# Kernel tuning notes

Measured on AMD Instinct MI355X. Metric: run time of the kernel, lower is better.

The kernel has to match this reference:

```python
import jax, jax.numpy as jnp
import numpy as np

N_NODES = 100000


def _deg_norm(idx, n):
    # inverse-sqrt degree, zero-degree nodes -> 0 (DGL norm='both' convention)
    deg = jax.ops.segment_sum(jnp.ones(idx.shape, jnp.float32), idx, num_segments=n)
    return jnp.where(deg > 0, jax.lax.rsqrt(jnp.maximum(deg, 1.0)), 0.0)


def graph_conv(x, src, dst, W, b, n):
    # symmetric normalization: D_out^{-1/2} on src, D_in^{-1/2} on dst
    norm_src = _deg_norm(src, n)  # [N]
    norm_dst = _deg_norm(dst, n)  # [N]
    h = (x * norm_src[:, None]) @ W          # apply weight first (in >= out)
    msg = h[src]                              # gather [E, out]
    agg = jax.ops.segment_sum(msg, dst, num_segments=n)  # scatter-add [N, out]
    return agg * norm_dst[:, None] + b


def setup_inputs() -> dict:
    key = jax.random.key(0)
    ks = jax.random.split(key, 6)
    x = jax.random.normal(ks[0], (N_NODES, 128), dtype=jnp.float32)
    edge_index = jax.random.randint(ks[1], (2, 1600000), 0, N_NODES, dtype=jnp.int64)
    W1 = jax.random.normal(ks[2], (128, 64), dtype=jnp.float32) * (1.0 / np.sqrt(128))
    b1 = jnp.zeros((64,), jnp.float32)
    W2 = jax.random.normal(ks[3], (64, 32), dtype=jnp.float32) * (1.0 / np.sqrt(64))
    b2 = jnp.zeros((32,), jnp.float32)
    Wl = jax.random.normal(ks[4], (32, 1), dtype=jnp.float32) * (1.0 / np.sqrt(32))
    bl = jnp.zeros((1,), jnp.float32)
    return {"x": x, "edge_index": edge_index, "W1": W1, "b1": b1,
            "W2": W2, "b2": b2, "Wl": Wl, "bl": bl}


def reference(x, edge_index, W1, b1, W2, b2, Wl, bl):
    src, dst = edge_index[0], edge_index[1]
    n = x.shape[0]
    h = graph_conv(x, src, dst, W1, b1, n)
    h = jax.nn.relu(h)
    # dropout(p=0.5) is identity at inference
    h = graph_conv(h, src, dst, W2, b2, n)
    return h @ Wl + bl  # [N, 1]
```

## Files before the change

kernel.cpp:

```cpp
#include <hip/hip_runtime.h>
#include <hip/hip_fp16.h>


#define WAVE 64
#define NRANGE 8

__global__ __launch_bounds__(256) void k_hist(const int* __restrict__ srcArr,
                                              const int* __restrict__ dstArr,
                                              unsigned* __restrict__ partial_s,
                                              unsigned* __restrict__ partial_d,
                                              int E, int B, int C, int chunkE) {
    extern __shared__ unsigned hist[];
    const int r = blockIdx.x & (NRANGE - 1);
    const int c = blockIdx.x >> 3;
    const int lo = r * B;
    const int* nodes = blockIdx.y ? dstArr : srcArr;
    unsigned* partial = blockIdx.y ? partial_d : partial_s;

    for (int b = threadIdx.x; b < B; b += 256) hist[b] = 0u;
    __syncthreads();

    const int beg = c * chunkE, end = min(beg + chunkE, E);
    const int n4 = (end - beg) >> 2;
    const int4* p = (const int4*)(nodes + beg);
    for (int j = threadIdx.x; j < n4; j += 256) {
        int4 v = p[j];
        int a;
        a = v.x - lo; if ((unsigned)a < (unsigned)B) atomicAdd(&hist[a], 1u);
        a = v.y - lo; if ((unsigned)a < (unsigned)B) atomicAdd(&hist[a], 1u);
        a = v.z - lo; if ((unsigned)a < (unsigned)B) atomicAdd(&hist[a], 1u);
        a = v.w - lo; if ((unsigned)a < (unsigned)B) atomicAdd(&hist[a], 1u);
    }
    for (int j = beg + (n4 << 2) + threadIdx.x; j < end; j += 256) {
        int a = nodes[j] - lo;
        if ((unsigned)a < (unsigned)B) atomicAdd(&hist[a], 1u);
    }
    __syncthreads();
    unsigned* outp = partial + (size_t)(r * C + c) * B;
    for (int b = threadIdx.x; b < B; b += 256) outp[b] = hist[b];
}

__global__ __launch_bounds__(256) void k_reduce_norm(const unsigned* __restrict__ partial_s,
                                                     unsigned* __restrict__ partial_d,
                                                     float* __restrict__ norm_s,
                                                     float* __restrict__ norm_d,
                                                     unsigned* __restrict__ deg_d,
                                                     int N, int B, int C) {
    int i = blockIdx.x * 256 + threadIdx.x;
    if (i >= N) return;
    int r = i / B, b = i - r * B;
    size_t base = (size_t)r * C * B + b;
    unsigned ds = 0;
    for (int c = 0; c < C; ++c) ds += partial_s[base + (size_t)c * B];
    unsigned dd = 0;
    for (int c = 0; c < C; ++c) {
        size_t ix = base + (size_t)c * B;
        unsigned v = partial_d[ix];
        partial_d[ix] = dd;
        dd += v;
    }
    deg_d[i] = dd;
    norm_s[i] = ds ? rsqrtf((float)ds) : 0.0f;
    norm_d[i] = dd ? rsqrtf((float)dd) : 0.0f;
}

__global__ void k_w2l(const float* __restrict__ W2, const float* __restrict__ b2,
                      const float* __restrict__ Wl, const float* __restrict__ bl,
                      float* __restrict__ w2l, float* __restrict__ c0) {
    int c = threadIdx.x;
    float acc = 0.f;
#pragma unroll
    for (int j = 0; j < 32; ++j) acc += W2[c * 32 + j] * Wl[j];
    w2l[c] = acc;
    if (c == 0) {
        float s = 0.f;
#pragma unroll
        for (int j = 0; j < 32; ++j) s += b2[j] * Wl[j];
        *c0 = s + bl[0];
    }
}

__global__ __launch_bounds__(256) void k_blocksum(const unsigned* __restrict__ deg,
                                                  unsigned* __restrict__ partial, int N) {
    __shared__ unsigned sw[4];
    int i = blockIdx.x * 256 + threadIdx.x;
    unsigned v = (i < N) ? deg[i] : 0u;
#pragma unroll
    for (int off = 32; off; off >>= 1) v += __shfl_xor((int)v, off);
    if ((threadIdx.x & 63) == 0) sw[threadIdx.x >> 6] = v;
    __syncthreads();
    if (threadIdx.x == 0) partial[blockIdx.x] = sw[0] + sw[1] + sw[2] + sw[3];
}

__global__ __launch_bounds__(512) void k_scanpartial(const unsigned* __restrict__ partial,
                                                     unsigned* __restrict__ blockoff,
                                                     unsigned* __restrict__ offsets,
                                                     int nb, int N) {
    __shared__ unsigned s[512];
    int t = threadIdx.x;
    unsigned v = (t < nb) ? partial[t] : 0u;
    s[t] = v;
    __syncthreads();
    for (int off = 1; off < 512; off <<= 1) {
        unsigned a = (t >= off) ? s[t - off] : 0u;
        __syncthreads();
        s[t] += a;
        __syncthreads();
    }
    if (t < nb) blockoff[t] = s[t] - v;
    if (t == nb - 1) offsets[N] = s[t];
}

__global__ __launch_bounds__(256) void k_offsets(const unsigned* __restrict__ deg,
                                                 const unsigned* __restrict__ blockoff,
                                                 unsigned* __restrict__ offsets, int N) {
    __shared__ unsigned s[256];
    int t = threadIdx.x;
    int i = blockIdx.x * 256 + t;
    unsigned v = (i < N) ? deg[i] : 0u;
    s[t] = v;
    __syncthreads();
    for (int off = 1; off < 256; off <<= 1) {
        unsigned a = (t >= off) ? s[t - off] : 0u;
        __syncthreads();
        s[t] += a;
        __syncthreads();
    }
    if (i < N) offsets[i] = blockoff[blockIdx.x] + s[t] - v;
}

__global__ __launch_bounds__(256) void k_fill(const int* __restrict__ src,
                                              const int* __restrict__ dst,
                                              const unsigned* __restrict__ offsets,
                                              const unsigned* __restrict__ rel,
                                              unsigned* __restrict__ csr,
                                              int N, int E, int B, int C, int chunkE) {
    extern __shared__ unsigned curs[];
    const int r = blockIdx.x & (NRANGE - 1);
    const int c = blockIdx.x >> 3;
    const int lo = r * B;
    const int bins = min(B, N - lo);
    const unsigned* relp = rel + (size_t)(r * C + c) * B;
    for (int b = threadIdx.x; b < bins; b += 256)
        curs[b] = offsets[lo + b] + relp[b];
    __syncthreads();

    const int beg = c * chunkE, end = min(beg + chunkE, E);
    const int n4 = (end - beg) >> 2;
    const int4* pd = (const int4*)(dst + beg);
    const int4* ps = (const int4*)(src + beg);
    for (int j = threadIdx.x; j < n4; j += 256) {
        int4 d4 = pd[j];
        int4 s4 = ps[j];
        int a;
        a = d4.x - lo; if ((unsigned)a < (unsigned)bins) csr[atomicAdd(&curs[a], 1u)] = (unsigned)s4.x;
        a = d4.y - lo; if ((unsigned)a < (unsigned)bins) csr[atomicAdd(&curs[a], 1u)] = (unsigned)s4.y;
        a = d4.z - lo; if ((unsigned)a < (unsigned)bins) csr[atomicAdd(&curs[a], 1u)] = (unsigned)s4.z;
        a = d4.w - lo; if ((unsigned)a < (unsigned)bins) csr[atomicAdd(&curs[a], 1u)] = (unsigned)s4.w;
    }
    for (int j = beg + (n4 << 2) + threadIdx.x; j < end; j += 256) {
        int a = dst[j] - lo;
        if ((unsigned)a < (unsigned)bins) csr[atomicAdd(&curs[a], 1u)] = (unsigned)src[j];
    }
}

__global__ __launch_bounds__(256) void k_gemm1(const float* __restrict__ x,
                                               const float* __restrict__ W1,
                                               const float* __restrict__ norm_s,
                                               __half* __restrict__ h1h, int N) {
    __shared__ float xT[64][65];
    __shared__ __align__(16) float Ws[64][64];
    const int tid = threadIdx.x;
    const int tx = tid & 15;
    const int ty = tid >> 4;
    const int r0 = blockIdx.x * 64;

    float acc[4][4] = {};

#pragma unroll
    for (int kt = 0; kt < 2; ++kt) {
#pragma unroll
        for (int it = 0; it < 16; ++it) {
            int e = it * 256 + tid;
            int r = e >> 6, k = e & 63;
            int row = r0 + r;
            float v = 0.f;
            if (row < N) v = x[(size_t)row * 128 + kt * 64 + k];
            xT[k][r] = v;
        }
#pragma unroll
        for (int it = 0; it < 16; ++it) {
            int e = it * 256 + tid;
            int k = e >> 6, cc = e & 63;
            Ws[k][cc] = W1[(size_t)(kt * 64 + k) * 64 + cc];
        }
        __syncthreads();
#pragma unroll 8
        for (int k = 0; k < 64; ++k) {
            float4 wv = *(const float4*)&Ws[k][tx * 4];
            float x0 = xT[k][ty * 4 + 0];
            float x1 = xT[k][ty * 4 + 1];
            float x2 = xT[k][ty * 4 + 2];
            float x3 = xT[k][ty * 4 + 3];
            acc[0][0] = fmaf(x0, wv.x, acc[0][0]); acc[0][1] = fmaf(x0, wv.y, acc[0][1]);
            acc[0][2] = fmaf(x0, wv.z, acc[0][2]); acc[0][3] = fmaf(x0, wv.w, acc[0][3]);
            acc[1][0] = fmaf(x1, wv.x, acc[1][0]); acc[1][1] = fmaf(x1, wv.y, acc[1][1]);
            acc[1][2] = fmaf(x1, wv.z, acc[1][2]); acc[1][3] = fmaf(x1, wv.w, acc[1][3]);
            acc[2][0] = fmaf(x2, wv.x, acc[2][0]); acc[2][1] = fmaf(x2, wv.y, acc[2][1]);
            acc[2][2] = fmaf(x2, wv.z, acc[2][2]); acc[2][3] = fmaf(x2, wv.w, acc[2][3]);
            acc[3][0] = fmaf(x3, wv.x, acc[3][0]); acc[3][1] = fmaf(x3, wv.y, acc[3][1]);
            acc[3][2] = fmaf(x3, wv.z, acc[3][2]); acc[3][3] = fmaf(x3, wv.w, acc[3][3]);
        }
        __syncthreads();
    }

#pragma unroll
    for (int i = 0; i < 4; ++i) {
        int row = r0 + ty * 4 + i;
        if (row < N) {
            float ns = norm_s[row];
            __half2 lo = __floats2half2_rn(acc[i][0] * ns, acc[i][1] * ns);
            __half2 hi = __floats2half2_rn(acc[i][2] * ns, acc[i][3] * ns);
            uint2 pk;
            pk.x = *(unsigned*)&lo;
            pk.y = *(unsigned*)&hi;
            *(uint2*)&h1h[(size_t)row * 64 + tx * 4] = pk;
        }
    }
}

__global__ __launch_bounds__(256) void k_agg_rdot(const unsigned* __restrict__ offsets,
                                                  const unsigned* __restrict__ csr,
                                                  const __half* __restrict__ h1h,
                                                  const float* __restrict__ norm_s,
                                                  const float* __restrict__ norm_d,
                                                  const float* __restrict__ b1,
                                                  const float* __restrict__ w2l,
                                                  float* __restrict__ s_node, int N) {
    const int lane = threadIdx.x & 63;
    const int slot = lane >> 5;
    const int p = lane & 31;
    const int v = (blockIdx.x * 256 + threadIdx.x) >> 6;
    if (v >= N) return;
    const unsigned beg = offsets[v], end = offsets[v + 1];

    float ax = 0.f, ay = 0.f;
    for (unsigned base = beg; base < end; base += WAVE) {
        const int n = (int)min((unsigned)WAVE, end - base);
        int sv = (lane < n) ? (int)csr[base + lane] : 0;
        int i = 0;
        for (; i + 8 <= n; i += 8) {
            int s0 = __shfl(sv, i + 0 + slot);
            int s1 = __shfl(sv, i + 2 + slot);
            int s2 = __shfl(sv, i + 4 + slot);
            int s3 = __shfl(sv, i + 6 + slot);
            unsigned u0 = *(const unsigned*)&h1h[(size_t)s0 * 64 + 2 * p];
            unsigned u1 = *(const unsigned*)&h1h[(size_t)s1 * 64 + 2 * p];
            unsigned u2 = *(const unsigned*)&h1h[(size_t)s2 * 64 + 2 * p];
            unsigned u3 = *(const unsigned*)&h1h[(size_t)s3 * 64 + 2 * p];
            float2 f0 = __half22float2(*(__half2*)&u0);
            float2 f1 = __half22float2(*(__half2*)&u1);
            float2 f2 = __half22float2(*(__half2*)&u2);
            float2 f3 = __half22float2(*(__half2*)&u3);
            ax += (f0.x + f1.x) + (f2.x + f3.x);
            ay += (f0.y + f1.y) + (f2.y + f3.y);
        }
        for (; i < n; i += 2) {
            int e = i + slot;
            int s = __shfl(sv, min(e, n - 1));
            if (e < n) {
                unsigned u = *(const unsigned*)&h1h[(size_t)s * 64 + 2 * p];
                float2 f = __half22float2(*(__half2*)&u);
                ax += f.x; ay += f.y;
            }
        }
    }
    ax += __shfl_xor(ax, 32);
    ay += __shfl_xor(ay, 32);

    float nd = norm_d[v];
    float t = fmaxf(fmaf(ax, nd, b1[2 * p]), 0.f) * w2l[2 * p]
            + fmaxf(fmaf(ay, nd, b1[2 * p + 1]), 0.f) * w2l[2 * p + 1];
#pragma unroll
    for (int off = 16; off; off >>= 1) t += __shfl_xor(t, off);
    if (lane == 0) s_node[v] = t * norm_s[v];
}

__global__ __launch_bounds__(256) void k_out(const unsigned* __restrict__ offsets,
                                             const unsigned* __restrict__ csr,
                                             const float* __restrict__ s_node,
                                             const float* __restrict__ norm_d,
                                             const float* __restrict__ c0,
                                             float* __restrict__ out, int N) {
    int v = blockIdx.x * 256 + threadIdx.x;
    if (v >= N) return;
    unsigned beg = offsets[v], end = offsets[v + 1];
    float sum = 0.f;
    unsigned j = beg;
    for (; j + 4 <= end; j += 4) {
        float a = s_node[csr[j + 0]], b = s_node[csr[j + 1]];
        float c = s_node[csr[j + 2]], d = s_node[csr[j + 3]];
        sum += a + b + c + d;
    }
    for (; j < end; ++j) sum += s_node[csr[j]];
    out[v] = fmaf(sum, norm_d[v], *c0);
}

extern "C" void kernel_launch(void* const* d_in, const int* in_sizes, int n_in,
                              void* d_out, int out_size, void* d_ws, size_t ws_size,
                              hipStream_t stream) {
    const float* x  = (const float*)d_in[0];
    const int*   ei = (const int*)d_in[1];
    const float* W1 = (const float*)d_in[2];
    const float* b1 = (const float*)d_in[3];
    const float* W2 = (const float*)d_in[4];
    const float* b2 = (const float*)d_in[5];
    const float* Wl = (const float*)d_in[6];
    const float* bl = (const float*)d_in[7];

    const int N = in_sizes[0] / 128;
    const int E = in_sizes[1] / 2;
    const int* src = ei;
    const int* dst = ei + E;
    const int NB = (N + 255) / 256;
    const int B = (N + NRANGE - 1) / NRANGE;

    size_t baseBytes = 0;
    {
        auto pad = [](size_t b) { return (b + 255) & ~(size_t)255; };
        baseBytes = pad((size_t)N * 4) * 3 + pad((size_t)(N + 1) * 4) +
                    pad((size_t)NB * 4) * 2 + pad((size_t)N * 64 * 2) +
                    pad((size_t)E * 4) + pad((size_t)N * 4) + pad(64 * 4) + pad(4);
    }
    int C = 32;
    while (C > 4 && baseBytes + 2ull * NRANGE * C * B * 4ull > ws_size) C >>= 1;
    const int chunkE = (((E + C - 1) / C) + 3) & ~3;

    char* w = (char*)d_ws;
    auto alloc = [&](size_t bytes) -> void* {
        void* r = (void*)w;
        w += (bytes + 255) & ~(size_t)255;
        return r;
    };
    float*    norm_s    = (float*)alloc((size_t)N * 4);
    float*    norm_d    = (float*)alloc((size_t)N * 4);
    unsigned* deg_d     = (unsigned*)alloc((size_t)N * 4);
    unsigned* offsets   = (unsigned*)alloc((size_t)(N + 1) * 4);
    unsigned* partial   = (unsigned*)alloc((size_t)NB * 4);
    unsigned* blockoff  = (unsigned*)alloc((size_t)NB * 4);
    __half*   h1h       = (__half*)alloc((size_t)N * 64 * 2);
    unsigned* csr       = (unsigned*)alloc((size_t)E * 4);
    float*    s_node    = (float*)alloc((size_t)N * 4);
    float*    w2l       = (float*)alloc(64 * 4);
    float*    c0        = (float*)alloc(4);
    unsigned* partial_s = (unsigned*)alloc((size_t)NRANGE * C * B * 4);
    unsigned* partial_d = (unsigned*)alloc((size_t)NRANGE * C * B * 4);

    float* out = (float*)d_out;
    const size_t ldsB = (size_t)B * 4;

    k_hist<<<dim3(NRANGE * C, 2), 256, ldsB, stream>>>(src, dst, partial_s, partial_d,
                                                       E, B, C, chunkE);
    k_w2l<<<1, 64, 0, stream>>>(W2, b2, Wl, bl, w2l, c0);
    k_reduce_norm<<<NB, 256, 0, stream>>>(partial_s, partial_d, norm_s, norm_d,
                                          deg_d, N, B, C);

    k_blocksum<<<NB, 256, 0, stream>>>(deg_d, partial, N);
    k_scanpartial<<<1, 512, 0, stream>>>(partial, blockoff, offsets, NB, N);
    k_offsets<<<NB, 256, 0, stream>>>(deg_d, blockoff, offsets, N);

    k_fill<<<NRANGE * C, 256, ldsB, stream>>>(src, dst, offsets, partial_d, csr,
                                              N, E, B, C, chunkE);

    k_gemm1<<<(N + 63) / 64, 256, 0, stream>>>(x, W1, norm_s, h1h, N);

    k_agg_rdot<<<(N + 3) / 4, 256, 0, stream>>>(offsets, csr, h1h, norm_s, norm_d,
                                                b1, w2l, s_node, N);
    k_out<<<NB, 256, 0, stream>>>(offsets, csr, s_node, norm_d, c0, out, N);
}
```

Baseline: 207.8 us.

## Use fp16 MFMA for first-layer GEMM with pre-transposed half weights

Replaces the scalar FP32 register-tiled GEMM for x@W1 with MFMA 16x16x32 f16 instructions. A new tiny kernel converts W1 to a transposed fp16 buffer, and x tiles are converted to fp16 and stored in an XOR-swizzled LDS layout to avoid bank conflicts. This is meant to cut the compute and LDS cost of the dense layer, but it rounds the inputs to fp16, which adds error, and adds one extra small launch. Output stores are now scalar half writes rather than packed ones.

```diff
diff --git a/kernel.cpp b/kernel.cpp
--- a/kernel.cpp
+++ b/kernel.cpp
@@ -4,6 +4,9 @@
 
 #define WAVE 64
 #define NRANGE 8
+
+typedef _Float16 f16x8 __attribute__((ext_vector_type(8)));
+typedef float f32x4 __attribute__((ext_vector_type(4)));
 
 __global__ __launch_bounds__(256) void k_hist(const int* __restrict__ srcArr,
                                               const int* __restrict__ dstArr,
@@ -80,6 +83,16 @@
     }
 }
 
+__global__ __launch_bounds__(256) void k_wt(const float* __restrict__ W1,
+                                            _Float16* __restrict__ wt) {
+    int t = threadIdx.x;
+    for (int i = 0; i < 32; ++i) {
+        int e = i * 256 + t;
+        int k = e >> 6, n = e & 63;
+        wt[n * 128 + k] = (_Float16)W1[e];
+    }
+}
+
 __global__ __launch_bounds__(256) void k_blocksum(const unsigned* __restrict__ deg,
                                                   unsigned* __restrict__ partial, int N) {
     __shared__ unsigned sw[4];
@@ -165,66 +178,60 @@
 }
 
 __global__ __launch_bounds__(256) void k_gemm1(const float* __restrict__ x,
-                                               const float* __restrict__ W1,
+                                               const _Float16* __restrict__ wt,
                                                const float* __restrict__ norm_s,
                                                __half* __restrict__ h1h, int N) {
-    __shared__ float xT[64][65];
-    __shared__ __align__(16) float Ws[64][64];
-    const int tid = threadIdx.x;
-    const int tx = tid & 15;
-    const int ty = tid >> 4;
+    __shared__ __align__(16) _Float16 xs[64 * 128];
+    const int tid = threadIdx.x, lane = tid & 63, wv = tid >> 6;
     const int r0 = blockIdx.x * 64;
 
-    float acc[4][4] = {};
-
-#pragma unroll
-    for (int kt = 0; kt < 2; ++kt) {
-#pragma unroll
-        for (int it = 0; it < 16; ++it) {
-            int e = it * 256 + tid;
-            int r = e >> 6, k = e & 63;
-            int row = r0 + r;
-            float v = 0.f;
-            if (row < N) v = x[(size_t)row * 128 + kt * 64 + k];
-            xT[k][r] = v;
-        }
-#pragma unroll
-        for (int it = 0; it < 16; ++it) {
-            int e = it * 256 + tid;
-            int k = e >> 6, cc = e & 63;
-            Ws[k][cc] = W1[(size_t)(kt * 64 + k) * 64 + cc];
-        }
-        __syncthreads();
-#pragma unroll 8
-        for (int k = 0; k < 64; ++k) {
-            float4 wv = *(const float4*)&Ws[k][tx * 4];
-            float x0 = xT[k][ty * 4 + 0];
-            float x1 = xT[k][ty * 4 + 1];
-            float x2 = xT[k][ty * 4 + 2];
-            float x3 = xT[k][ty * 4 + 3];
-            acc[0][0] = fmaf(x0, wv.x, acc[0][0]); acc[0][1] = fmaf(x0, wv.y, acc[0][1]);
-            acc[0][2] = fmaf(x0, wv.z, acc[0][2]); acc[0][3] = fmaf(x0, wv.w, acc[0][3]);
-            acc[1][0] = fmaf(x1, wv.x, acc[1][0]); acc[1][1] = fmaf(x1, wv.y, acc[1][1]);
-            acc[1][2] = fmaf(x1, wv.z, acc[1][2]); acc[1][3] = fmaf(x1, wv.w, acc[1][3]);
-            acc[2][0] = fmaf(x2, wv.x, acc[2][0]); acc[2][1] = fmaf(x2, wv.y, acc[2][1]);
-            acc[2][2] = fmaf(x2, wv.z, acc[2][2]); acc[2][3] = fmaf(x2, wv.w, acc[2][3]);
-            acc[3][0] = fmaf(x3, wv.x, acc[3][0]); acc[3][1] = fmaf(x3, wv.y, acc[3][1]);
-            acc[3][2] = fmaf(x3, wv.z, acc[3][2]); acc[3][3] = fmaf(x3, wv.w, acc[3][3]);
-        }
-        __syncthreads();
-    }
-
-#pragma unroll
-    for (int i = 0; i < 4; ++i) {
-        int row = r0 + ty * 4 + i;
+    f16x8 bf[4][4];
+#pragma unroll
+    for (int kt = 0; kt < 4; ++kt)
+#pragma unroll
+        for (int nt = 0; nt < 4; ++nt)
+            bf[kt][nt] = *(const f16x8*)&wt[(nt * 16 + (lane & 15)) * 128 +
+                                            kt * 32 + (lane >> 4) * 8];
+
+#pragma unroll
+    for (int it = 0; it < 8; ++it) {
+        int e = it * 256 + tid;
+        int r = e >> 5, c = e & 31;
+        int row = r0 + r;
+        float4 v = (row < N) ? ((const float4*)x)[(size_t)row * 32 + c]
+                             : make_float4(0.f, 0.f, 0.f, 0.f);
+        __half2 lo2 = __floats2half2_rn(v.x, v.y);
+        __half2 hi2 = __floats2half2_rn(v.z, v.w);
+        uint2 pk;
+        pk.x = *(unsigned*)&lo2;
+        pk.y = *(unsigned*)&hi2;
+        int byte = r * 256 + c * 8;
+        byte ^= (r & 7) << 4;
+        *(uint2*)((char*)xs + byte) = pk;
+    }
+    __syncthreads();
+
+    f32x4 acc[4] = {};
+    const int rloc = wv * 16 + (lane & 15);
+#pragma unroll
+    for (int kt = 0; kt < 4; ++kt) {
+        int byte = rloc * 256 + (kt * 32 + (lane >> 4) * 8) * 2;
+        byte ^= (rloc & 7) << 4;
+        f16x8 af = *(const f16x8*)((char*)xs + byte);
+#pragma unroll
+        for (int nt = 0; nt < 4; ++nt)
+            acc[nt] = __builtin_amdgcn_mfma_f32_16x16x32_f16(af, bf[kt][nt], acc[nt], 0, 0, 0);
+    }
+
+#pragma unroll
+    for (int j = 0; j < 4; ++j) {
+        int row = r0 + wv * 16 + (lane >> 4) * 4 + j;
         if (row < N) {
             float ns = norm_s[row];
-            __half2 lo = __floats2half2_rn(acc[i][0] * ns, acc[i][1] * ns);
-            __half2 hi = __floats2half2_rn(acc[i][2] * ns, acc[i][3] * ns);
-            uint2 pk;
-            pk.x = *(unsigned*)&lo;
-            pk.y = *(unsigned*)&hi;
-            *(uint2*)&h1h[(size_t)row * 64 + tx * 4] = pk;
+#pragma unroll
+            for (int nt = 0; nt < 4; ++nt)
+                h1h[(size_t)row * 64 + nt * 16 + (lane & 15)] =
+                    __float2half(acc[nt][j] * ns);
         }
     }
 }
@@ -330,7 +337,8 @@
         auto pad = [](size_t b) { return (b + 255) & ~(size_t)255; };
         baseBytes = pad((size_t)N * 4) * 3 + pad((size_t)(N + 1) * 4) +
                     pad((size_t)NB * 4) * 2 + pad((size_t)N * 64 * 2) +
-                    pad((size_t)E * 4) + pad((size_t)N * 4) + pad(64 * 4) + pad(4);
+                    pad((size_t)E * 4) + pad((size_t)N * 4) + pad(64 * 4) + pad(4) +
+                    pad(64 * 128 * 2);
     }
     int C = 32;
     while (C > 4 && baseBytes + 2ull * NRANGE * C * B * 4ull > ws_size) C >>= 1;
@@ -353,6 +361,7 @@
     float*    s_node    = (float*)alloc((size_t)N * 4);
     float*    w2l       = (float*)alloc(64 * 4);
     float*    c0        = (float*)alloc(4);
+    _Float16* wt        = (_Float16*)alloc(64 * 128 * 2);
     unsigned* partial_s = (unsigned*)alloc((size_t)NRANGE * C * B * 4);
     unsigned* partial_d = (unsigned*)alloc((size_t)NRANGE * C * B * 4);
 
@@ -362,6 +371,7 @@
     k_hist<<<dim3(NRANGE * C, 2), 256, ldsB, stream>>>(src, dst, partial_s, partial_d,
                                                        E, B, C, chunkE);
     k_w2l<<<1, 64, 0, stream>>>(W2, b2, Wl, bl, w2l, c0);
+    k_wt<<<1, 256, 0, stream>>>(W1, wt);
     k_reduce_norm<<<NB, 256, 0, stream>>>(partial_s, partial_d, norm_s, norm_d,
                                           deg_d, N, B, C);
 
@@ -372,7 +382,7 @@
     k_fill<<<NRANGE * C, 256, ldsB, stream>>>(src, dst, offsets, partial_d, csr,
                                               N, E, B, C, chunkE);
 
-    k_gemm1<<<(N + 63) / 64, 256, 0, stream>>>(x, W1, norm_s, h1h, N);
+    k_gemm1<<<(N + 63) / 64, 256, 0, stream>>>(x, wt, norm_s, h1h, N);
 
     k_agg_rdot<<<(N + 3) / 4, 256, 0, stream>>>(offsets, csr, h1h, norm_s, norm_d,
                                                 b1, w2l, s_node, N);
```

Result: faster. 196.3 us (-5.5%).
